# Performance work log

Hardware: AMD Instinct MI355X
Metric: run time of the kernel (lower is better)

Reference implementation:

```python
import jax, jax.numpy as jnp
import numpy as np

HEADS = 8
C = 256            # in_channels == out_channels
NUM_STAR = 4
G = 32             # num graphs
N = 100000         # num nodes
LN_EPS = 1e-5


def setup_inputs() -> dict:
    key = jax.random.key(0)
    ks = jax.random.split(key, 9)
    stars = jax.random.normal(ks[0], (G, NUM_STAR, C), jnp.float32)
    nodes = jax.random.normal(ks[1], (N, C), jnp.float32)
    batch = jnp.sort(jax.random.randint(ks[2], (N,), 0, G))
    s = 1.0 / np.sqrt(C).astype(np.float32)
    Wq_w = jax.random.normal(ks[3], (C, C), jnp.float32) * s
    Wk_w = jax.random.normal(ks[4], (C, C), jnp.float32) * s
    Wv_w = jax.random.normal(ks[5], (C, C), jnp.float32) * s
    Wq_b = jnp.zeros((C,), jnp.float32)
    Wk_b = jnp.zeros((C,), jnp.float32)
    Wv_b = jnp.zeros((C,), jnp.float32)
    ln_gamma = jnp.ones((C,), jnp.float32)
    ln_beta = jnp.zeros((C,), jnp.float32)
    return dict(stars=stars, nodes=nodes, batch=batch,
                Wq_w=Wq_w, Wq_b=Wq_b, Wk_w=Wk_w, Wk_b=Wk_b,
                Wv_w=Wv_w, Wv_b=Wv_b, ln_gamma=ln_gamma, ln_beta=ln_beta)


def reference(stars, nodes, batch, Wq_w, Wq_b, Wk_w, Wk_b, Wv_w, Wv_b, ln_gamma, ln_beta):
    g, num_star, c = stars.shape
    n = nodes.shape[0]
    h = HEADS
    dh = c // h
    s_total = g * num_star                       # number of star nodes
    num_seg = n + s_total

    # x = [nodes; flattened stars]  (star index of (graph gidx, star i) = n + num_star*gidx + i)
    x = jnp.concatenate([nodes, stars.reshape(-1, c)], axis=0)     # [n+S, c]
    q = (x @ Wq_w.T + Wq_b).reshape(-1, h, dh)
    k = (x @ Wk_w.T + Wk_b).reshape(-1, h, dh)
    v = (x @ Wv_w.T + Wv_b).reshape(-1, h, dh)

    # edges: every node -> each of its graph's stars, plus star self-loops (use_star=True)
    rows = (n + num_star * batch[None, :] + jnp.arange(num_star)[:, None]).reshape(-1)  # [num_star*n]
    cols = jnp.broadcast_to(jnp.arange(n), (num_star, n)).reshape(-1)
    star_idx = jnp.arange(n, n + s_total)
    ei = jnp.concatenate([rows, star_idx])       # targets (query side)
    ej = jnp.concatenate([cols, star_idx])       # sources (key/value side)

    qe = q[ei]                                   # [E, h, dh]
    ke = k[ej]
    ve = v[ej]

    score = jnp.einsum('ehd,ehd->eh', qe, ke) / np.sqrt(dh).astype(np.float32)

    # segment softmax over target index (PyG-style, +1e-16 in denominator)
    m = jax.ops.segment_max(score, ei, num_segments=num_seg)
    m = jnp.where(jnp.isfinite(m), m, 0.0)       # empty segments -> 0
    ex = jnp.exp(score - m[ei])
    denom = jax.ops.segment_sum(ex, ei, num_segments=num_seg)
    coef = ex / (denom[ei] + 1e-16)              # [E, h]

    # dropout is identity in eval mode
    out = jax.ops.segment_sum(ve * coef[:, :, None], ei, num_segments=num_seg)  # [n+S, h, dh]
    new_stars = out[n:].reshape(g, num_star, c)

    new_stars = jax.nn.elu(new_stars)            # activation
    new_stars = new_stars + stars                # residual

    mu = jnp.mean(new_stars, axis=-1, keepdims=True)
    var = jnp.mean(jnp.square(new_stars - mu), axis=-1, keepdims=True)
    new_stars = (new_stars - mu) / jnp.sqrt(var + LN_EPS) * ln_gamma + ln_beta
    return new_stars
```

## Files before the change

kernel.cpp:

```cpp
#include <hip/hip_runtime.h>
#include <math.h>

#define HEADS 8
#define C 256
#define NUM_STAR 4
#define SLOTS 32
#define RSQRT_DH 0.17677669529663688f
#define LN_EPS 1e-5f
#define PF 16
#define NT 32
#define FS 260
#define EP2 40

typedef __attribute__((ext_vector_type(8))) short short8;
typedef __attribute__((ext_vector_type(4))) float floatx4;

typedef const unsigned int __attribute__((address_space(1)))* gp1_t;
typedef unsigned int __attribute__((address_space(3)))* lp3_t;

__device__ __forceinline__ unsigned int f2b(float f) {
    unsigned int u = __float_as_uint(f);
    return (u + 0x7fffu + ((u >> 16) & 1u)) >> 16;
}
__device__ __forceinline__ float b2f(unsigned short v) {
    return __uint_as_float(((unsigned int)v) << 16);
}
__device__ __forceinline__ unsigned int pk_bf16(float lo, float hi) {
    unsigned int r;
    asm("v_cvt_pk_bf16_f32 %0, %1, %2" : "=v"(r) : "v"(lo), "v"(hi));
    return r;
}
__device__ __forceinline__ void gld_lds16(const float* g, float* l) {
    __builtin_amdgcn_global_load_lds((gp1_t)(const void*)g, (lp3_t)(void*)l, 16, 0, 0);
}
__device__ __forceinline__ void block_sync_lds() {
    asm volatile("s_waitcnt lgkmcnt(0)" ::: "memory");
    __builtin_amdgcn_sched_barrier(0);
    __builtin_amdgcn_s_barrier();
    __builtin_amdgcn_sched_barrier(0);
}

__global__ void k_star_prep(const float* __restrict__ stars,
                            const float* __restrict__ Wq_w, const float* __restrict__ Wq_b,
                            const float* __restrict__ Wk_w, const float* __restrict__ Wk_b,
                            unsigned short* __restrict__ U16, float* __restrict__ eself,
                            float* __restrict__ denom,
                            const int* __restrict__ batch, int N, int G,
                            int* __restrict__ gstart) {
    if (blockIdx.x == gridDim.x - 1) {
        int g = threadIdx.x;
        if (g > G) return;
        if (g == 0) { gstart[0] = 0; return; }
        if (g == G) { gstart[G] = N; return; }
        int lo = 0, hi = N;
        while (lo < hi) {
            int mid = (lo + hi) >> 1;
            if (batch[mid] < g) lo = mid + 1; else hi = mid;
        }
        gstart[g] = lo;
        return;
    }

    __shared__ float xs[C];
    __shared__ float qv[C];
    __shared__ float kv[C];
    const int gs = blockIdx.x;
    const int g = gs >> 2, s = gs & 3;
    const int t = threadIdx.x;

    xs[t] = stars[gs * C + t];
    __syncthreads();

    float aq = Wq_b[t], ak = Wk_b[t];
    const float* wq = Wq_w + (size_t)t * C;
    const float* wk = Wk_w + (size_t)t * C;
    #pragma unroll 4
    for (int j = 0; j < C; j += 4) {
        float4 x4 = *(const float4*)(xs + j);
        float4 a4 = *(const float4*)(wq + j);
        aq += a4.x * x4.x + a4.y * x4.y + a4.z * x4.z + a4.w * x4.w;
        float4 b4 = *(const float4*)(wk + j);
        ak += b4.x * x4.x + b4.y * x4.y + b4.z * x4.z + b4.w * x4.w;
    }
    qv[t] = aq; kv[t] = ak;
    __syncthreads();

    {
        float p = qv[t] * kv[t];
        #pragma unroll
        for (int off = 16; off; off >>= 1) p += __shfl_down(p, off, 32);
        if ((t & 31) == 0) {
            int h = t >> 5;
            float e = __expf(p * RSQRT_DH);
            eself[g * SLOTS + s * HEADS + h] = e;
            denom[g * SLOTS + s * HEADS + h] = e;
        }
    }

    {
        const int c = t;
        #pragma unroll
        for (int h = 0; h < HEADS; ++h) {
            float u = 0.f;
            #pragma unroll
            for (int d = 0; d < 32; ++d)
                u += Wk_w[(size_t)(h * 32 + d) * C + c] * qv[h * 32 + d];
            U16[((size_t)g * SLOTS + s * HEADS + h) * C + c] =
                (unsigned short)f2b(u * RSQRT_DH);
        }
    }
}

__global__ __launch_bounds__(256, 2)
void k_fused(const float* __restrict__ nodes, const unsigned short* __restrict__ U16,
             const int* __restrict__ gstart, float* __restrict__ denom,
             unsigned short* __restrict__ Ypart16) {
    __shared__ float          fbuf[2][NT][FS];
    __shared__ unsigned short el[SLOTS * EP2];

    const int g = blockIdx.x / PF, pb = blockIdx.x % PF;
    const int t = threadIdx.x;
    const int wv = t >> 6;
    const int l  = t & 63;
    const int lr = l & 15;
    const int q  = l >> 4;
    const int st = wv & 1;
    const int ng = wv >> 1;

    const int glo = gstart[g], ghi = gstart[g + 1];
    const int len = ghi - glo;
    const int Lb = (len + PF - 1) / PF;
    const int blo = glo + pb * Lb;
    const int bhi = min(blo + Lb, ghi);
    const int nrw = (bhi > blo) ? (bhi - blo + NT - 1) / NT : 0;

    const floatx4 z4 = {0.f, 0.f, 0.f, 0.f};
    floatx4 yacc[2][4];
    #pragma unroll
    for (int a = 0; a < 2; ++a)
        #pragma unroll
        for (int b = 0; b < 4; ++b) yacc[a][b] = z4;
    float dsum[4];
    #pragma unroll
    for (int i = 0; i < 4; ++i) dsum[i] = 0.f;

    if (nrw > 0) {
        short8 ureg[8];
        {
            const unsigned short* ug = U16 + (size_t)g * SLOTS * C;
            #pragma unroll
            for (int kt = 0; kt < 8; ++kt)
                ureg[kt] = *(const short8*)&ug[(st * 16 + lr) * C + q * 8 + kt * 32];
        }
        asm volatile("s_waitcnt vmcnt(0)" ::: "memory");

        auto issue = [&](int r) {
            const int buf = r & 1;
            #pragma unroll
            for (int i = 0; i < 8; ++i) {
                int row = wv * 8 + i;
                int gn = blo + r * NT + row;
                if (gn >= bhi) gn = blo;
                gld_lds16(nodes + (size_t)gn * C + l * 4, &fbuf[buf][row][0]);
            }
        };

        issue(0);
        issue(1);

        for (int rd = 0; rd < nrw; ++rd) {
            const int cur = rd & 1;
            asm volatile("s_waitcnt vmcnt(8)" ::: "memory");
            __builtin_amdgcn_sched_barrier(0);
            __builtin_amdgcn_s_barrier();
            __builtin_amdgcn_sched_barrier(0);

            floatx4 sacc = z4;
            {
                const float* xr = &fbuf[cur][ng * 16 + lr][q * 8];
                #pragma unroll
                for (int kt = 0; kt < 8; ++kt) {
                    float4 a4 = *(const float4*)(xr + kt * 32);
                    float4 b4 = *(const float4*)(xr + kt * 32 + 4);
                    short8 bx;
                    ((unsigned int*)&bx)[0] = pk_bf16(a4.x, a4.y);
                    ((unsigned int*)&bx)[1] = pk_bf16(a4.z, a4.w);
                    ((unsigned int*)&bx)[2] = pk_bf16(b4.x, b4.y);
                    ((unsigned int*)&bx)[3] = pk_bf16(b4.z, b4.w);
                    sacc = __builtin_amdgcn_mfma_f32_16x16x32_bf16(ureg[kt], bx, sacc, 0, 0, 0);
                }
            }
            {
                const bool valid = (blo + rd * NT + ng * 16 + lr) < bhi;
                #pragma unroll
                for (int r = 0; r < 4; ++r) {
                    float ev = valid ? __expf(sacc[r]) : 0.f;
                    dsum[r] += ev;
                    el[(st * 16 + q * 4 + r) * EP2 + ng * 16 + lr] = (unsigned short)f2b(ev);
                }
            }
            block_sync_lds();

            {
                short8 pa0 = *(const short8*)&el[lr * EP2 + q * 8];
                short8 pa1 = *(const short8*)&el[(16 + lr) * EP2 + q * 8];
                #pragma unroll
                for (int ct = 0; ct < 4; ++ct) {
                    const int c = wv * 64 + ct * 16 + lr;
                    short8 bx;
                    const float* col = &fbuf[cur][q * 8][c];
                    ((unsigned int*)&bx)[0] = pk_bf16(col[0 * FS], col[1 * FS]);
                    ((unsigned int*)&bx)[1] = pk_bf16(col[2 * FS], col[3 * FS]);
                    ((unsigned int*)&bx)[2] = pk_bf16(col[4 * FS], col[5 * FS]);
                    ((unsigned int*)&bx)[3] = pk_bf16(col[6 * FS], col[7 * FS]);
                    yacc[0][ct] = __builtin_amdgcn_mfma_f32_16x16x32_bf16(pa0, bx, yacc[0][ct], 0, 0, 0);
                    yacc[1][ct] = __builtin_amdgcn_mfma_f32_16x16x32_bf16(pa1, bx, yacc[1][ct], 0, 0, 0);
                }
            }
            block_sync_lds();
            issue(rd + 2);
        }

        asm volatile("s_waitcnt vmcnt(0)" ::: "memory");

        #pragma unroll
        for (int i = 0; i < 4; ++i) {
            float v = dsum[i];
            v += __shfl_xor(v, 1);
            v += __shfl_xor(v, 2);
            v += __shfl_xor(v, 4);
            v += __shfl_xor(v, 8);
            dsum[i] = v;
        }
        if (lr == 0) {
            #pragma unroll
            for (int r = 0; r < 4; ++r)
                atomicAdd(&denom[g * SLOTS + st * 16 + q * 4 + r], dsum[r]);
        }
    }

    {
        unsigned short* yg = &Ypart16[(((size_t)g * PF + pb) * SLOTS) * C];
        #pragma unroll
        for (int st2 = 0; st2 < 2; ++st2)
            #pragma unroll
            for (int ct = 0; ct < 4; ++ct)
                #pragma unroll
                for (int r = 0; r < 4; ++r)
                    yg[(st2 * 16 + q * 4 + r) * C + wv * 64 + ct * 16 + lr] =
                        (unsigned short)f2b(yacc[st2][ct][r]);
    }
}

__global__ void k_epilogue(const float* __restrict__ stars,
                           const float* __restrict__ Wv_w, const float* __restrict__ Wv_b,
                           const float* __restrict__ gamma, const float* __restrict__ beta,
                           const unsigned short* __restrict__ Ypart16,
                           const float* __restrict__ eself,
                           const float* __restrict__ denom, float* __restrict__ out) {
    __shared__ float xs[C];
    __shared__ float yl[HEADS * C];
    __shared__ float cs[HEADS], ivd[HEADS], scl[HEADS];
    __shared__ float rb[8];

    const int gs = blockIdx.x;
    const int g = gs >> 2, s = gs & 3;
    const int t = threadIdx.x;

    xs[t] = stars[gs * C + t];
    if (t < HEADS) {
        float dn = denom[g * SLOTS + s * HEADS + t];
        float iv = 1.f / (dn + 1e-16f);
        ivd[t] = iv;
        cs[t] = eself[g * SLOTS + s * HEADS + t] * iv;
        scl[t] = dn * iv;
    }
    __syncthreads();

    for (int i = t; i < HEADS * C; i += 256) {
        int h = i >> 8, j = i & 255;
        float sum = 0.f;
        #pragma unroll
        for (int pbi = 0; pbi < PF; ++pbi)
            sum += b2f(Ypart16[(((size_t)g * PF + pbi) * SLOTS + s * HEADS + h) * C + j]);
        yl[i] = sum * ivd[h] + cs[h] * xs[j];
    }
    __syncthreads();

    const int c = t, h = c >> 5;
    float a = 0.f;
    const float* wv = Wv_w + (size_t)c * C;
    const float* yh = &yl[h * C];
    #pragma unroll 4
    for (int j = 0; j < C; j += 4) {
        float4 w4 = *(const float4*)(wv + j);
        float4 y4 = *(const float4*)(yh + j);
        a += w4.x * y4.x + w4.y * y4.y + w4.z * y4.z + w4.w * y4.w;
    }
    a += Wv_b[c] * scl[h];

    float v = a > 0.f ? a : (__expf(a) - 1.f);
    float r = v + xs[c];

    float ssum = r;
    #pragma unroll
    for (int off = 32; off; off >>= 1) ssum += __shfl_down(ssum, off, 64);
    const int wid = t >> 6, lane = t & 63;
    if (lane == 0) rb[wid] = ssum;
    __syncthreads();
    const float mu = (rb[0] + rb[1] + rb[2] + rb[3]) * (1.f / 256.f);
    const float d = r - mu;
    float vsum = d * d;
    #pragma unroll
    for (int off = 32; off; off >>= 1) vsum += __shfl_down(vsum, off, 64);
    if (lane == 0) rb[4 + wid] = vsum;
    __syncthreads();
    const float var = (rb[4] + rb[5] + rb[6] + rb[7]) * (1.f / 256.f);
    out[gs * C + c] = d * rsqrtf(var + LN_EPS) * gamma[c] + beta[c];
}

extern "C" void kernel_launch(void* const* d_in, const int* in_sizes, int n_in,
                              void* d_out, int out_size, void* d_ws, size_t ws_size,
                              hipStream_t stream) {
    const float* stars = (const float*)d_in[0];
    const float* nodes = (const float*)d_in[1];
    const int*   batch = (const int*)d_in[2];
    const float* Wq_w  = (const float*)d_in[3];
    const float* Wq_b  = (const float*)d_in[4];
    const float* Wk_w  = (const float*)d_in[5];
    const float* Wk_b  = (const float*)d_in[6];
    const float* Wv_w  = (const float*)d_in[7];
    const float* Wv_b  = (const float*)d_in[8];
    const float* gamma = (const float*)d_in[9];
    const float* beta  = (const float*)d_in[10];

    const int N = in_sizes[1] / C;
    const int G = in_sizes[0] / (NUM_STAR * C);

    unsigned short* U16 = (unsigned short*)d_ws;
    float* eself = (float*)((char*)d_ws + (size_t)G * SLOTS * C * 2);
    float* denom = eself + (size_t)G * SLOTS;
    unsigned short* Ypart16 = (unsigned short*)(denom + (size_t)G * SLOTS);
    int*   gstart = (int*)(Ypart16 + (size_t)G * PF * SLOTS * C);

    float* out = (float*)d_out;

    k_star_prep<<<G * NUM_STAR + 1, 256, 0, stream>>>(stars, Wq_w, Wq_b, Wk_w, Wk_b,
                                                      U16, eself, denom,
                                                      batch, N, G, gstart);
    k_fused<<<G * PF, 256, 0, stream>>>(nodes, U16, gstart, denom, Ypart16);
    k_epilogue<<<G * NUM_STAR, 256, 0, stream>>>(stars, Wv_w, Wv_b, gamma, beta,
                                                 Ypart16, eself, denom, out);
}
```

Measured before the change: 65.56 us.

## Warp-specialize fused kernel into score and value producer/consumer wave groups

```diff
diff --git a/kernel.cpp b/kernel.cpp
--- a/kernel.cpp
+++ b/kernel.cpp
@@ -7,7 +7,7 @@
 #define SLOTS 32
 #define RSQRT_DH 0.17677669529663688f
 #define LN_EPS 1e-5f
-#define PF 16
+#define PF 8
 #define NT 32
 #define FS 260
 #define EP2 40
@@ -111,12 +111,12 @@
     }
 }
 
-__global__ __launch_bounds__(256, 2)
+__global__ __launch_bounds__(512, 1)
 void k_fused(const float* __restrict__ nodes, const unsigned short* __restrict__ U16,
              const int* __restrict__ gstart, float* __restrict__ denom,
              unsigned short* __restrict__ Ypart16) {
-    __shared__ float          fbuf[2][NT][FS];
-    __shared__ unsigned short el[SLOTS * EP2];
+    __shared__ float          fbuf[4][NT][FS];
+    __shared__ unsigned short el[2][SLOTS * EP2];
 
     const int g = blockIdx.x / PF, pb = blockIdx.x % PF;
     const int t = threadIdx.x;
@@ -125,7 +125,7 @@
     const int lr = l & 15;
     const int q  = l >> 4;
     const int st = wv & 1;
-    const int ng = wv >> 1;
+    const int ng = (wv >> 1) & 1;
 
     const int glo = gstart[g], ghi = gstart[g + 1];
     const int len = ghi - glo;
@@ -146,7 +146,7 @@
 
     if (nrw > 0) {
         short8 ureg[8];
-        {
+        if (wv < 4) {
             const unsigned short* ug = U16 + (size_t)g * SLOTS * C;
             #pragma unroll
             for (int kt = 0; kt < 8; ++kt)
@@ -155,10 +155,10 @@
         asm volatile("s_waitcnt vmcnt(0)" ::: "memory");
 
         auto issue = [&](int r) {
-            const int buf = r & 1;
-            #pragma unroll
-            for (int i = 0; i < 8; ++i) {
-                int row = wv * 8 + i;
+            const int buf = r & 3;
+            #pragma unroll
+            for (int i = 0; i < 4; ++i) {
+                int row = wv * 4 + i;
                 int gn = blo + r * NT + row;
                 if (gn >= bhi) gn = blo;
                 gld_lds16(nodes + (size_t)gn * C + l * 4, &fbuf[buf][row][0]);
@@ -168,47 +168,53 @@
         issue(0);
         issue(1);
 
-        for (int rd = 0; rd < nrw; ++rd) {
-            const int cur = rd & 1;
-            asm volatile("s_waitcnt vmcnt(8)" ::: "memory");
-            __builtin_amdgcn_sched_barrier(0);
-            __builtin_amdgcn_s_barrier();
-            __builtin_amdgcn_sched_barrier(0);
-
-            floatx4 sacc = z4;
-            {
-                const float* xr = &fbuf[cur][ng * 16 + lr][q * 8];
-                #pragma unroll
-                for (int kt = 0; kt < 8; ++kt) {
-                    float4 a4 = *(const float4*)(xr + kt * 32);
-                    float4 b4 = *(const float4*)(xr + kt * 32 + 4);
-                    short8 bx;
-                    ((unsigned int*)&bx)[0] = pk_bf16(a4.x, a4.y);
-                    ((unsigned int*)&bx)[1] = pk_bf16(a4.z, a4.w);
-                    ((unsigned int*)&bx)[2] = pk_bf16(b4.x, b4.y);
-                    ((unsigned int*)&bx)[3] = pk_bf16(b4.z, b4.w);
-                    sacc = __builtin_amdgcn_mfma_f32_16x16x32_bf16(ureg[kt], bx, sacc, 0, 0, 0);
+        for (int rd = 0; rd <= nrw; ++rd) {
+            if (rd < nrw) {
+                asm volatile("s_waitcnt vmcnt(4)" ::: "memory");
+                __builtin_amdgcn_sched_barrier(0);
+            }
+            block_sync_lds();
+
+            if (rd < nrw) {
+                issue(rd + 2);
+
+                if (wv < 4) {
+                    floatx4 sacc = z4;
+                    {
+                        const float* xr = &fbuf[rd & 3][ng * 16 + lr][q * 8];
+                        #pragma unroll
+                        for (int kt = 0; kt < 8; ++kt) {
+                            float4 a4 = *(const float4*)(xr + kt * 32);
+                            float4 b4 = *(const float4*)(xr + kt * 32 + 4);
+                            short8 bx;
+                            ((unsigned int*)&bx)[0] = pk_bf16(a4.x, a4.y);
+                            ((unsigned int*)&bx)[1] = pk_bf16(a4.z, a4.w);
+                            ((unsigned int*)&bx)[2] = pk_bf16(b4.x, b4.y);
+                            ((unsigned int*)&bx)[3] = pk_bf16(b4.z, b4.w);
+                            sacc = __builtin_amdgcn_mfma_f32_16x16x32_bf16(ureg[kt], bx, sacc, 0, 0, 0);
+                        }
+                    }
+                    const bool valid = (blo + rd * NT + ng * 16 + lr) < bhi;
+                    unsigned short* ew = el[rd & 1];
+                    #pragma unroll
+                    for (int r = 0; r < 4; ++r) {
+                        float ev = valid ? __expf(sacc[r]) : 0.f;
+                        dsum[r] += ev;
+                        ew[(st * 16 + q * 4 + r) * EP2 + ng * 16 + lr] = (unsigned short)f2b(ev);
+                    }
                 }
             }
-            {
-                const bool valid = (blo + rd * NT + ng * 16 + lr) < bhi;
-                #pragma unroll
-                for (int r = 0; r < 4; ++r) {
-                    float ev = valid ? __expf(sacc[r]) : 0.f;
-                    dsum[r] += ev;
-                    el[(st * 16 + q * 4 + r) * EP2 + ng * 16 + lr] = (unsigned short)f2b(ev);
-                }
-            }
-            block_sync_lds();
-
-            {
-                short8 pa0 = *(const short8*)&el[lr * EP2 + q * 8];
-                short8 pa1 = *(const short8*)&el[(16 + lr) * EP2 + q * 8];
+
+            if (rd >= 1 && wv >= 4) {
+                const unsigned short* ep = el[(rd - 1) & 1];
+                const float (*fb)[FS] = fbuf[(rd - 1) & 3];
+                short8 pa0 = *(const short8*)&ep[lr * EP2 + q * 8];
+                short8 pa1 = *(const short8*)&ep[(16 + lr) * EP2 + q * 8];
                 #pragma unroll
                 for (int ct = 0; ct < 4; ++ct) {
-                    const int c = wv * 64 + ct * 16 + lr;
+                    const int c = (wv - 4) * 64 + ct * 16 + lr;
                     short8 bx;
-                    const float* col = &fbuf[cur][q * 8][c];
+                    const float* col = &fb[q * 8][c];
                     ((unsigned int*)&bx)[0] = pk_bf16(col[0 * FS], col[1 * FS]);
                     ((unsigned int*)&bx)[1] = pk_bf16(col[2 * FS], col[3 * FS]);
                     ((unsigned int*)&bx)[2] = pk_bf16(col[4 * FS], col[5 * FS]);
@@ -217,37 +223,43 @@
                     yacc[1][ct] = __builtin_amdgcn_mfma_f32_16x16x32_bf16(pa1, bx, yacc[1][ct], 0, 0, 0);
                 }
             }
-            block_sync_lds();
-            issue(rd + 2);
         }
 
         asm volatile("s_waitcnt vmcnt(0)" ::: "memory");
 
-        #pragma unroll
-        for (int i = 0; i < 4; ++i) {
-            float v = dsum[i];
-            v += __shfl_xor(v, 1);
-            v += __shfl_xor(v, 2);
-            v += __shfl_xor(v, 4);
-            v += __shfl_xor(v, 8);
-            dsum[i] = v;
-        }
-        if (lr == 0) {
-            #pragma unroll
-            for (int r = 0; r < 4; ++r)
-                atomicAdd(&denom[g * SLOTS + st * 16 + q * 4 + r], dsum[r]);
-        }
-    }
-
-    {
+        if (wv < 4) {
+            #pragma unroll
+            for (int i = 0; i < 4; ++i) {
+                float v = dsum[i];
+                v += __shfl_xor(v, 1);
+                v += __shfl_xor(v, 2);
+                v += __shfl_xor(v, 4);
+                v += __shfl_xor(v, 8);
+                dsum[i] = v;
+            }
+            if (lr == 0 && ng == 0) {
+                #pragma unroll
+                for (int r = 0; r < 4; ++r)
+                    atomicAdd(&denom[g * SLOTS + st * 16 + q * 4 + r], dsum[r]);
+            }
+            if (lr == 0 && ng == 1) {
+                #pragma unroll
+                for (int r = 0; r < 4; ++r)
+                    atomicAdd(&denom[g * SLOTS + st * 16 + q * 4 + r], dsum[r]);
+            }
+        }
+    }
+
+    if (wv >= 4) {
         unsigned short* yg = &Ypart16[(((size_t)g * PF + pb) * SLOTS) * C];
+        const int cw = (wv - 4) * 64;
         #pragma unroll
         for (int st2 = 0; st2 < 2; ++st2)
             #pragma unroll
             for (int ct = 0; ct < 4; ++ct)
                 #pragma unroll
                 for (int r = 0; r < 4; ++r)
-                    yg[(st2 * 16 + q * 4 + r) * C + wv * 64 + ct * 16 + lr] =
+                    yg[(st2 * 16 + q * 4 + r) * C + cw + ct * 16 + lr] =
                         (unsigned short)f2b(yacc[st2][ct][r]);
     }
 }
@@ -348,7 +360,7 @@
     k_star_prep<<<G * NUM_STAR + 1, 256, 0, stream>>>(stars, Wq_w, Wq_b, Wk_w, Wk_b,
                                                       U16, eself, denom,
                                                       batch, N, G, gstart);
-    k_fused<<<G * PF, 256, 0, stream>>>(nodes, U16, gstart, denom, Ypart16);
+    k_fused<<<G * PF, 512, 0, stream>>>(nodes, U16, gstart, denom, Ypart16);
     k_epilogue<<<G * NUM_STAR, 256, 0, stream>>>(stars, Wv_w, Wv_b, gamma, beta,
                                                  Ypart16, eself, denom, out);
 }
```

Measured after the change: 64.09 us. 2.2% less time.
